# Kernel optimization log

Measured on AMD Instinct MI355X. Metric: run time of the kernel, lower is better.

## Reference

```python
import jax, jax.numpy as jnp
import numpy as np

D = 2048      # hidden_size
H = 16        # num_heads
DH = D // H   # head_dim
DFF = 8192    # intermediate_size
EPS = 1e-6


def setup_inputs() -> dict:
    key = jax.random.key(0)
    ks = jax.random.split(key, 12)
    s = 0.02
    return {
        "x": jax.random.normal(ks[0], (2, 2048, D), dtype=jnp.float32),
        "wq": jax.random.normal(ks[1], (D, D), dtype=jnp.float32) * s,
        "bq": jnp.zeros((D,), dtype=jnp.float32),
        "wk": jax.random.normal(ks[2], (D, D), dtype=jnp.float32) * s,
        "bk": jnp.zeros((D,), dtype=jnp.float32),
        "wv": jax.random.normal(ks[3], (D, D), dtype=jnp.float32) * s,
        "bv": jnp.zeros((D,), dtype=jnp.float32),
        "wo": jax.random.normal(ks[4], (D, D), dtype=jnp.float32) * s,
        "bo": jnp.zeros((D,), dtype=jnp.float32),
        "w_gate": jax.random.normal(ks[5], (DFF, D), dtype=jnp.float32) * s,
        "w_up": jax.random.normal(ks[6], (DFF, D), dtype=jnp.float32) * s,
        "w_down": jax.random.normal(ks[7], (D, DFF), dtype=jnp.float32) * s,
        "g_att": jnp.ones((D,), dtype=jnp.float32),
        "g_ffn": jnp.ones((D,), dtype=jnp.float32),
    }


def _rmsnorm(x, w):
    # Faithful to source: multiplies by sqrt(mean(x^2)+eps) (source bug kept).
    var = jnp.mean(x * x, axis=-1, keepdims=True)
    return x * jnp.sqrt(var + EPS) * w


def _mha(x, wq, bq, wk, bk, wv, bv, wo, bo):
    B, S, _ = x.shape
    def split(t):  # [B,S,D] -> [B,H,S,DH]
        return t.reshape(B, S, H, DH).transpose(0, 2, 1, 3)
    q = split(x @ wq.T + bq)
    k = split(x @ wk.T + bk)
    v = split(x @ wv.T + bv)
    scores = jnp.einsum("bhsd,bhtd->bhst", q, k) / jnp.sqrt(jnp.float32(DH))
    probs = jax.nn.softmax(scores, axis=-1)
    out = jnp.einsum("bhst,bhtd->bhsd", probs, v)       # [B,H,S,DH]
    # Faithful quirk: transpose(-1,-2) (NOT (1,2)), then view(B,-1,D)
    out = out.transpose(0, 1, 3, 2).reshape(B, S, D)    # scrambled layout, as in source
    return out @ wo.T + bo


def _ffn(x, w_gate, w_up, w_down):
    inter = jax.nn.relu(x @ w_gate.T) * (x @ w_up.T)
    return inter @ w_down.T


def reference(x, wq, bq, wk, bk, wv, bv, wo, bo, w_gate, w_up, w_down, g_att, g_ffn):
    h = x + _mha(_rmsnorm(x, g_att), wq, bq, wk, bk, wv, bv, wo, bo)
    out = h + _ffn(_rmsnorm(h, g_ffn), w_gate, w_up, w_down)
    return out
```

## Files before the change

kernel.cpp:

```cpp
#include <hip/hip_runtime.h>

typedef __attribute__((ext_vector_type(8))) short short8;
typedef __attribute__((ext_vector_type(4))) float f32x4;
typedef __attribute__((ext_vector_type(4))) unsigned short us4;
typedef unsigned short u16;

__device__ __forceinline__ u16 f2bf(float f) {
    unsigned u = __builtin_bit_cast(unsigned, f);
    return (u16)((u + 0x7fffu + ((u >> 16) & 1u)) >> 16);
}
__device__ __forceinline__ float bf2f(u16 h) {
    unsigned u = ((unsigned)h) << 16;
    return __builtin_bit_cast(float, u);
}
__device__ __forceinline__ void async16(const void* g, void* l) {
    __builtin_amdgcn_global_load_lds((const __attribute__((address_space(1))) unsigned int*)g,
                                     (__attribute__((address_space(3))) unsigned int*)l,
                                     16, 0, 0);
}

__global__ __launch_bounds__(256) void cvt_k(const float* __restrict__ in, u16* __restrict__ out) {
    int i = (blockIdx.x * 256 + threadIdx.x) * 4;
    f32x4 v = *(const f32x4*)(in + i);
    us4 o;
    o[0] = f2bf(v[0]); o[1] = f2bf(v[1]); o[2] = f2bf(v[2]); o[3] = f2bf(v[3]);
    *(us4*)(out + i) = o;
}

__global__ __launch_bounds__(256) void rmsnorm_k(const float* __restrict__ X, const float* __restrict__ g,
                                                 u16* __restrict__ O) {
    const int row = blockIdx.x, tid = threadIdx.x;
    const float* xr = X + (long)row * 2048 + tid * 8;
    f32x4 v0 = *(const f32x4*)xr;
    f32x4 v1 = *(const f32x4*)(xr + 4);
    float ss = v0[0]*v0[0] + v0[1]*v0[1] + v0[2]*v0[2] + v0[3]*v0[3]
             + v1[0]*v1[0] + v1[1]*v1[1] + v1[2]*v1[2] + v1[3]*v1[3];
#pragma unroll
    for (int m = 1; m < 64; m <<= 1) ss += __shfl_xor(ss, m, 64);
    __shared__ float wsum[4];
    if ((tid & 63) == 0) wsum[tid >> 6] = ss;
    __syncthreads();
    float tot = wsum[0] + wsum[1] + wsum[2] + wsum[3];
    const float sc = sqrtf(tot * (1.0f / 2048.0f) + 1e-6f);
    const float* gr = g + tid * 8;
    f32x4 g0 = *(const f32x4*)gr, g1 = *(const f32x4*)(gr + 4);
    us4 o0, o1;
    o0[0] = f2bf(v0[0] * sc * g0[0]); o0[1] = f2bf(v0[1] * sc * g0[1]);
    o0[2] = f2bf(v0[2] * sc * g0[2]); o0[3] = f2bf(v0[3] * sc * g0[3]);
    o1[0] = f2bf(v1[0] * sc * g1[0]); o1[1] = f2bf(v1[1] * sc * g1[1]);
    o1[2] = f2bf(v1[2] * sc * g1[2]); o1[3] = f2bf(v1[3] * sc * g1[3]);
    u16* op = O + (long)row * 2048 + tid * 8;
    *(us4*)op = o0;
    *(us4*)(op + 4) = o1;
}

enum { M_QKV = 0, M_VT = 1, M_H1 = 2, M_RELU = 3, M_MUL = 4, M_ADD = 5 };

template <int MODE, int BN>
__global__ __launch_bounds__(512, 2) void gemm8p(const u16* __restrict__ A, const u16* __restrict__ W,
                                                 const float* __restrict__ bias, const float* resid,
                                                 const u16* aux, void* out,
                                                 int N, int K, float scale) {
    constexpr int MF = BN / 32;
    constexpr int HF = MF / 2;
    constexpr int NF = 4;
    constexpr int BSLOT = BN * 32;
    __shared__ alignas(16) u16 As[2][2][8192];
    __shared__ alignas(16) u16 Bs[2][2][BSLOT];

    const int tid = threadIdx.x, wv = tid >> 6, lane = tid & 63;
    const int q4 = lane >> 4, lr = lane & 15;
    const int wm = (BN == 256) ? (wv >> 2) * 128 : (wv >> 1) * 64;
    const int wn = (BN == 256) ? (wv & 3) * 64 : (wv & 1) * 64;

    const int ntn = N / BN;
    int wg = blockIdx.x;
    {
        const int nwg = gridDim.x, q = nwg >> 3, r = nwg & 7, x = wg & 7, l = wg >> 3;
        wg = (x < r ? x * (q + 1) : r * (q + 1) + (x - r) * q) + l;
    }
    const long m0 = (long)(wg / ntn) * 256;
    const int n0 = (wg % ntn) * BN;

    const int cswz = (q4 ^ ((lr >> 1) & 3)) * 8;
    const int a_rd = (wm + lr) * 32 + cswz;
    const int b_rd = (wn + lr) * 32 + cswz;

    const int srow = tid >> 2;
    const int slc = ((tid & 3) ^ ((srow >> 1) & 3)) * 8;
    const u16* gA0 = A + (m0 + srow) * (long)K + slc;
    const u16* gA1 = gA0 + 128 * (long)K;
    const u16* gB0 = W + ((long)n0 + srow) * K + slc;
    const u16* gB1 = (BN == 256) ? gB0 + 128 * (long)K : gB0;

    f32x4 acc[MF][NF] = {};
    short8 bfr[NF];

#define STAGEA(BUF, KS, KOFF) do {                       \
        u16* d_ = &As[BUF][KS][wv * 512];                \
        async16(gA0 + (KOFF), d_);                       \
        async16(gA1 + (KOFF), d_ + 4096); } while (0)
#define STAGEB(BUF, KS, KOFF) do {                       \
        u16* d_ = &Bs[BUF][KS][wv * 512];                \
        async16(gB0 + (KOFF), d_);                       \
        if (BN == 256) async16(gB1 + (KOFF), d_ + 4096); } while (0)
#define VMW_N do { if (BN == 256) asm volatile("s_waitcnt vmcnt(6)" ::: "memory"); \
                   else           asm volatile("s_waitcnt vmcnt(4)" ::: "memory"); } while (0)
#define VMW_0 asm volatile("s_waitcnt vmcnt(0)" ::: "memory")
#define PHASE(BUF, KS, FSEL, STAGE_, VMW_) do {                                              \
        short8 afr_[HF];                                                                     \
        _Pragma("unroll") for (int m_ = 0; m_ < HF; m_++)                                    \
            afr_[m_] = *(const short8*)(&As[BUF][KS][a_rd + ((FSEL) * HF + m_) * 512]);      \
        if ((FSEL) == 0) {                                                                   \
            _Pragma("unroll") for (int n_ = 0; n_ < NF; n_++)                                \
                bfr[n_] = *(const short8*)(&Bs[BUF][KS][b_rd + n_ * 512]);                   \
        }                                                                                    \
        STAGE_;                                                                              \
        __builtin_amdgcn_s_barrier();                                                        \
        asm volatile("s_waitcnt lgkmcnt(0)");                                                \
        __builtin_amdgcn_s_setprio(1);                                                       \
        _Pragma("unroll") for (int m_ = 0; m_ < HF; m_++)                                    \
            _Pragma("unroll") for (int n_ = 0; n_ < NF; n_++)                                \
                acc[(FSEL) * HF + m_][n_] = __builtin_amdgcn_mfma_f32_16x16x32_bf16(         \
                    afr_[m_], bfr[n_], acc[(FSEL) * HF + m_][n_], 0, 0, 0);                  \
        __builtin_amdgcn_s_setprio(0);                                                       \
        VMW_;                                                                                \
        __builtin_amdgcn_sched_barrier(0);                                                   \
        __builtin_amdgcn_s_barrier();                                                        \
    } while (0)

    STAGEB(0, 0, 0);  STAGEA(0, 0, 0);  STAGEB(0, 1, 32); STAGEA(0, 1, 32);
    STAGEB(1, 0, 64); STAGEA(1, 0, 64); STAGEB(1, 1, 96);
    VMW_N;
    __builtin_amdgcn_s_barrier();

    const int NI = K >> 7;
    int k0 = 0;
    for (int i = 0; i < NI - 1; ++i, k0 += 128) {
        PHASE(0, 0, 0, STAGEA(1, 1, k0 + 96),  );
        PHASE(0, 0, 1, STAGEB(0, 0, k0 + 128), );
        PHASE(0, 1, 0, STAGEA(0, 0, k0 + 128), );
        PHASE(0, 1, 1, STAGEB(0, 1, k0 + 160), VMW_N);
        PHASE(1, 0, 0, STAGEA(0, 1, k0 + 160), );
        PHASE(1, 0, 1, STAGEB(1, 0, k0 + 192), );
        PHASE(1, 1, 0, STAGEA(1, 0, k0 + 192), );
        PHASE(1, 1, 1, STAGEB(1, 1, k0 + 224), VMW_N);
    }
    PHASE(0, 0, 0, STAGEA(1, 1, k0 + 96), );
    PHASE(0, 0, 1, , );
    PHASE(0, 1, 0, , );
    PHASE(0, 1, 1, , VMW_0);
    PHASE(1, 0, 0, , );
    PHASE(1, 0, 1, , );
    PHASE(1, 1, 0, , );
    PHASE(1, 1, 1, , );

#undef PHASE
#undef VMW_0
#undef VMW_N
#undef STAGEB
#undef STAGEA

#pragma unroll
    for (int m = 0; m < MF; m++) {
#pragma unroll
        for (int n = 0; n < NF; n++) {
            const int gn = n0 + wn + n * 16 + lr;
#pragma unroll
            for (int r = 0; r < 4; r++) {
                const long gm = m0 + wm + m * 16 + q4 * 4 + r;
                float v = acc[m][n][r];
                if constexpr (MODE == M_QKV) {
                    v = (v + bias[gn]) * scale;
                    ((u16*)out)[gm * N + gn] = f2bf(v);
                } else if constexpr (MODE == M_VT) {
                    v = v + bias[gm];
                    const long b = gn >> 11, s = gn & 2047;
                    ((u16*)out)[(b << 22) + gm * 2048 + s] = f2bf(v);
                } else if constexpr (MODE == M_H1) {
                    ((float*)out)[gm * N + gn] = v + bias[gn] + resid[gm * N + gn];
                } else if constexpr (MODE == M_RELU) {
                    ((u16*)out)[gm * N + gn] = f2bf(fmaxf(v, 0.0f));
                } else if constexpr (MODE == M_MUL) {
                    ((u16*)out)[gm * N + gn] = f2bf(v * bf2f(aux[gm * N + gn]));
                } else {
                    ((float*)out)[gm * N + gn] = v + resid[gm * N + gn];
                }
            }
        }
    }
}

__global__ __launch_bounds__(512) void attn_kernel(const u16* __restrict__ Q, const u16* __restrict__ Km,
                                                   const u16* __restrict__ Vt, u16* __restrict__ Oscr) {
    __shared__ u16 Ks[128 * 128];
    __shared__ u16 Vs[128 * 128];
    __shared__ u16 Ps[8][16 * 136];
    __shared__ float abuf[8][16];
    __shared__ float lbuf[8][16];
    const int tid = threadIdx.x, w = tid >> 6, lane = tid & 63;
    const int q4 = lane >> 4, lr = lane & 15;
    const int bh = blockIdx.y, b = bh >> 4, h = bh & 15;
    const int sw = blockIdx.x * 128 + w * 16;
    const long qkbase = ((long)b * 2048) * 2048 + h * 128;
    const long vtbase = ((long)b * 2048 + h * 128) * 2048;

    short8 qf[4];
    {
        const u16* qr = Q + qkbase + (long)(sw + lr) * 2048 + q4 * 8;
#pragma unroll
        for (int kk = 0; kk < 4; kk++) qf[kk] = *(const short8*)(qr + kk * 32);
    }
    float m_i[4], l_i[4];
#pragma unroll
    for (int r = 0; r < 4; r++) { m_i[r] = -1e30f; l_i[r] = 0.0f; }
    f32x4 oacc[8] = {};

    for (int t0 = 0; t0 < 2048; t0 += 128) {
        __syncthreads();
#pragma unroll
        for (int i = 0; i < 4; i++) {
            const int c = i * 512 + tid;
            const int row = c >> 4;
            const int lc = (c & 15) ^ (row & 15);
            async16(Km + qkbase + (long)(t0 + row) * 2048 + lc * 8, (u16*)Ks + (i * 512 + w * 64) * 8);
            async16(Vt + vtbase + (long)row * 2048 + t0 + lc * 8, (u16*)Vs + (i * 512 + w * 64) * 8);
        }
        __syncthreads();
        f32x4 sacc[8] = {};
#pragma unroll
        for (int kk = 0; kk < 4; kk++) {
#pragma unroll
            for (int n = 0; n < 8; n++) {
                const int pc = (kk * 4 + q4) ^ lr;
                short8 kf = *(const short8*)(Ks + ((n * 16 + lr) * 16 + pc) * 8);
                sacc[n] = __builtin_amdgcn_mfma_f32_16x16x32_bf16(qf[kk], kf, sacc[n], 0, 0, 0);
            }
        }
        float al[4];
#pragma unroll
        for (int r = 0; r < 4; r++) {
            float mx = sacc[0][r];
#pragma unroll
            for (int n = 1; n < 8; n++) mx = fmaxf(mx, sacc[n][r]);
#pragma unroll
            for (int msk = 1; msk < 16; msk <<= 1) mx = fmaxf(mx, __shfl_xor(mx, msk, 64));
            const float mn = fmaxf(m_i[r], mx);
            al[r] = __expf(m_i[r] - mn);
            float rs = 0.0f;
#pragma unroll
            for (int n = 0; n < 8; n++) {
                float p = __expf(sacc[n][r] - mn);
                sacc[n][r] = p;
                rs += p;
            }
#pragma unroll
            for (int msk = 1; msk < 16; msk <<= 1) rs += __shfl_xor(rs, msk, 64);
            l_i[r] = l_i[r] * al[r] + rs;
            m_i[r] = mn;
        }
#pragma unroll
        for (int n = 0; n < 8; n++)
#pragma unroll
            for (int r = 0; r < 4; r++)
                Ps[w][(q4 * 4 + r) * 136 + n * 16 + lr] = f2bf(sacc[n][r]);
        if (lr == 0) {
#pragma unroll
            for (int r = 0; r < 4; r++) abuf[w][q4 * 4 + r] = al[r];
        }
        __syncthreads();
        const float a_s = abuf[w][lr];
#pragma unroll
        for (int mm = 0; mm < 8; mm++) oacc[mm] *= a_s;
#pragma unroll
        for (int kk = 0; kk < 4; kk++) {
            short8 pf = *(const short8*)(&Ps[w][lr * 136 + kk * 32 + q4 * 8]);
            const int pc = (kk * 4 + q4) ^ lr;
#pragma unroll
            for (int mm = 0; mm < 8; mm++) {
                short8 vf = *(const short8*)(Vs + ((mm * 16 + lr) * 16 + pc) * 8);
                oacc[mm] = __builtin_amdgcn_mfma_f32_16x16x32_bf16(vf, pf, oacc[mm], 0, 0, 0);
            }
        }
    }
    if (lr == 0) {
#pragma unroll
        for (int r = 0; r < 4; r++) lbuf[w][q4 * 4 + r] = l_i[r];
    }
    __syncthreads();
    const float linv = 1.0f / lbuf[w][lr];
#pragma unroll
    for (int mm = 0; mm < 8; mm++) {
#pragma unroll
        for (int r = 0; r < 4; r++) {
            const int d = mm * 16 + q4 * 4 + r;
            Oscr[vtbase + (long)d * 2048 + sw + lr] = f2bf(oacc[mm][r] * linv);
        }
    }
}

extern "C" void kernel_launch(void* const* d_in, const int* in_sizes, int n_in,
                              void* d_out, int out_size, void* d_ws, size_t ws_size,
                              hipStream_t stream) {
    const float* x  = (const float*)d_in[0];
    const float* wq = (const float*)d_in[1];
    const float* bq = (const float*)d_in[2];
    const float* wk = (const float*)d_in[3];
    const float* bk = (const float*)d_in[4];
    const float* wv = (const float*)d_in[5];
    const float* bv = (const float*)d_in[6];
    const float* wo = (const float*)d_in[7];
    const float* bo = (const float*)d_in[8];
    const float* wg = (const float*)d_in[9];
    const float* wu = (const float*)d_in[10];
    const float* wd = (const float*)d_in[11];
    const float* ga = (const float*)d_in[12];
    const float* gf = (const float*)d_in[13];

    char* ws = (char*)d_ws;
    const size_t MB = (size_t)1 << 20;
    u16*  xn    = (u16*)(ws + 0);
    u16*  scr   = (u16*)(ws + 0);
    u16*  hn    = (u16*)(ws + 0);
    u16*  qb    = (u16*)(ws + 16 * MB);
    u16*  kb    = (u16*)(ws + 32 * MB);
    u16*  vt    = (u16*)(ws + 48 * MB);
    u16*  grelu = (u16*)(ws + 16 * MB);
    u16*  inter = grelu;
    u16*  wreg  = (u16*)(ws + 80 * MB);
    u16*  wq_b  = wreg;
    u16*  wk_b  = wreg + 4 * MB;
    u16*  wv_b  = wreg + 8 * MB;
    u16*  wo_b  = wreg + 12 * MB;
    u16*  wbig  = wreg;
    float* h1   = (float*)d_out;

    cvt_k<<<4096, 256, 0, stream>>>(wq, wq_b);
    cvt_k<<<4096, 256, 0, stream>>>(wk, wk_b);
    cvt_k<<<4096, 256, 0, stream>>>(wv, wv_b);
    cvt_k<<<4096, 256, 0, stream>>>(wo, wo_b);

    rmsnorm_k<<<4096, 256, 0, stream>>>(x, ga, xn);

    const float qscale = 0.08838834764831843f;
    gemm8p<M_QKV, 128><<<256, 512, 0, stream>>>(xn, wq_b, bq, nullptr, nullptr, qb, 2048, 2048, qscale);
    gemm8p<M_QKV, 128><<<256, 512, 0, stream>>>(xn, wk_b, bk, nullptr, nullptr, kb, 2048, 2048, 1.0f);
    gemm8p<M_VT, 128><<<256, 512, 0, stream>>>(wv_b, xn, bv, nullptr, nullptr, vt, 4096, 2048, 1.0f);

    attn_kernel<<<dim3(16, 32), 512, 0, stream>>>(qb, kb, vt, scr);

    gemm8p<M_H1, 128><<<256, 512, 0, stream>>>(scr, wo_b, bo, x, nullptr, h1, 2048, 2048, 1.0f);

    cvt_k<<<16384, 256, 0, stream>>>(wg, wbig);
    rmsnorm_k<<<4096, 256, 0, stream>>>(h1, gf, hn);

    gemm8p<M_RELU, 256><<<512, 512, 0, stream>>>(hn, wbig, nullptr, nullptr, nullptr, grelu, 8192, 2048, 1.0f);

    cvt_k<<<16384, 256, 0, stream>>>(wu, wbig);
    gemm8p<M_MUL, 256><<<512, 512, 0, stream>>>(hn, wbig, nullptr, nullptr, grelu, inter, 8192, 2048, 1.0f);

    cvt_k<<<16384, 256, 0, stream>>>(wd, wbig);
    gemm8p<M_ADD, 128><<<256, 512, 0, stream>>>(inter, wbig, nullptr, h1, nullptr, d_out, 2048, 8192, 1.0f);
}
```

Measured before the change: 1.126 ms.

## Restructure BN=128 GEMM pipeline into four full-K phases with joint A/B staging

For the BN=128 variant, each k-slice is now handled in one phase that does all four M fragments at once (HF fixed at 4), instead of two half-phases. A and B tiles for the same slice are staged together, with a per-phase vmcnt wait. This halves the number of barriers per k-iteration for that variant and gives each barrier more MFMA work. The cost is more A-fragment registers held live per phase and a shallower prefetch distance. The BN=256 path keeps its schedule, with an explicit read-B flag added.

```diff
diff --git a/kernel.cpp b/kernel.cpp
--- a/kernel.cpp
+++ b/kernel.cpp
@@ -62,7 +62,7 @@
                                                  const u16* aux, void* out,
                                                  int N, int K, float scale) {
     constexpr int MF = BN / 32;
-    constexpr int HF = MF / 2;
+    constexpr int HF = 4;
     constexpr int NF = 4;
     constexpr int BSLOT = BN * 32;
     __shared__ alignas(16) u16 As[2][2][8192];
@@ -104,14 +104,12 @@
         u16* d_ = &Bs[BUF][KS][wv * 512];                \
         async16(gB0 + (KOFF), d_);                       \
         if (BN == 256) async16(gB1 + (KOFF), d_ + 4096); } while (0)
-#define VMW_N do { if (BN == 256) asm volatile("s_waitcnt vmcnt(6)" ::: "memory"); \
-                   else           asm volatile("s_waitcnt vmcnt(4)" ::: "memory"); } while (0)
-#define VMW_0 asm volatile("s_waitcnt vmcnt(0)" ::: "memory")
-#define PHASE(BUF, KS, FSEL, STAGE_, VMW_) do {                                              \
+#define VM(N) asm volatile("s_waitcnt vmcnt(" #N ")" ::: "memory")
+#define PHASE(BUF, KS, FSEL, RDB, STAGE_, VMW_) do {                                         \
         short8 afr_[HF];                                                                     \
         _Pragma("unroll") for (int m_ = 0; m_ < HF; m_++)                                    \
             afr_[m_] = *(const short8*)(&As[BUF][KS][a_rd + ((FSEL) * HF + m_) * 512]);      \
-        if ((FSEL) == 0) {                                                                   \
+        if (RDB) {                                                                           \
             _Pragma("unroll") for (int n_ = 0; n_ < NF; n_++)                                \
                 bfr[n_] = *(const short8*)(&Bs[BUF][KS][b_rd + n_ * 512]);                   \
         }                                                                                    \
@@ -129,35 +127,51 @@
         __builtin_amdgcn_s_barrier();                                                        \
     } while (0)
 
-    STAGEB(0, 0, 0);  STAGEA(0, 0, 0);  STAGEB(0, 1, 32); STAGEA(0, 1, 32);
-    STAGEB(1, 0, 64); STAGEA(1, 0, 64); STAGEB(1, 1, 96);
-    VMW_N;
-    __builtin_amdgcn_s_barrier();
-
     const int NI = K >> 7;
     int k0 = 0;
-    for (int i = 0; i < NI - 1; ++i, k0 += 128) {
-        PHASE(0, 0, 0, STAGEA(1, 1, k0 + 96),  );
-        PHASE(0, 0, 1, STAGEB(0, 0, k0 + 128), );
-        PHASE(0, 1, 0, STAGEA(0, 0, k0 + 128), );
-        PHASE(0, 1, 1, STAGEB(0, 1, k0 + 160), VMW_N);
-        PHASE(1, 0, 0, STAGEA(0, 1, k0 + 160), );
-        PHASE(1, 0, 1, STAGEB(1, 0, k0 + 192), );
-        PHASE(1, 1, 0, STAGEA(1, 0, k0 + 192), );
-        PHASE(1, 1, 1, STAGEB(1, 1, k0 + 224), VMW_N);
-    }
-    PHASE(0, 0, 0, STAGEA(1, 1, k0 + 96), );
-    PHASE(0, 0, 1, , );
-    PHASE(0, 1, 0, , );
-    PHASE(0, 1, 1, , VMW_0);
-    PHASE(1, 0, 0, , );
-    PHASE(1, 0, 1, , );
-    PHASE(1, 1, 0, , );
-    PHASE(1, 1, 1, , );
+
+    if constexpr (BN == 256) {
+        STAGEB(0, 0, 0);  STAGEA(0, 0, 0);  STAGEB(0, 1, 32); STAGEA(0, 1, 32);
+        STAGEB(1, 0, 64); STAGEA(1, 0, 64); STAGEB(1, 1, 96);
+        VM(6);
+        __builtin_amdgcn_s_barrier();
+        for (int i = 0; i < NI - 1; ++i, k0 += 128) {
+            PHASE(0, 0, 0, 1, STAGEA(1, 1, k0 + 96),  );
+            PHASE(0, 0, 1, 0, STAGEB(0, 0, k0 + 128), );
+            PHASE(0, 1, 0, 1, STAGEA(0, 0, k0 + 128), );
+            PHASE(0, 1, 1, 0, STAGEB(0, 1, k0 + 160), VM(6));
+            PHASE(1, 0, 0, 1, STAGEA(0, 1, k0 + 160), );
+            PHASE(1, 0, 1, 0, STAGEB(1, 0, k0 + 192), );
+            PHASE(1, 1, 0, 1, STAGEA(1, 0, k0 + 192), );
+            PHASE(1, 1, 1, 0, STAGEB(1, 1, k0 + 224), VM(6));
+        }
+        PHASE(0, 0, 0, 1, STAGEA(1, 1, k0 + 96), );
+        PHASE(0, 0, 1, 0, , );
+        PHASE(0, 1, 0, 1, , );
+        PHASE(0, 1, 1, 0, , VM(0));
+        PHASE(1, 0, 0, 1, , );
+        PHASE(1, 0, 1, 0, , );
+        PHASE(1, 1, 0, 1, , );
+        PHASE(1, 1, 1, 0, , );
+    } else {
+        STAGEB(0, 0, 0);  STAGEA(0, 0, 0);  STAGEB(0, 1, 32); STAGEA(0, 1, 32);
+        STAGEB(1, 0, 64); STAGEA(1, 0, 64);
+        VM(6);
+        __builtin_amdgcn_s_barrier();
+        for (int i = 0; i < NI - 1; ++i, k0 += 128) {
+            PHASE(0, 0, 0, 1, do { STAGEA(1, 1, k0 + 96);  STAGEB(1, 1, k0 + 96);  } while (0), VM(6));
+            PHASE(0, 1, 0, 1, do { STAGEA(0, 0, k0 + 128); STAGEB(0, 0, k0 + 128); } while (0), VM(6));
+            PHASE(1, 0, 0, 1, do { STAGEA(0, 1, k0 + 160); STAGEB(0, 1, k0 + 160); } while (0), VM(6));
+            PHASE(1, 1, 0, 1, do { STAGEA(1, 0, k0 + 192); STAGEB(1, 0, k0 + 192); } while (0), VM(6));
+        }
+        PHASE(0, 0, 0, 1, do { STAGEA(1, 1, k0 + 96); STAGEB(1, 1, k0 + 96); } while (0), VM(6));
+        PHASE(0, 1, 0, 1, , VM(3));
+        PHASE(1, 0, 0, 1, , VM(0));
+        PHASE(1, 1, 0, 1, , );
+    }
 
 #undef PHASE
-#undef VMW_0
-#undef VMW_N
+#undef VM
 #undef STAGEB
 #undef STAGEA
 
```

After: 1.100 ms. 2.3% less time.
